# Kernel tuning notes

Measured on AMD Instinct MI355X. Metric: run time of the kernel, lower is better.

The kernel has to match this reference:

```python
import jax, jax.numpy as jnp
import numpy as np

NUM_CONCEPT = 256
NUM_QUESTION = 10000
DIM_EMB = 64
TIME_LOG = 5.0
BATCH, SEQ = 32, 1024


def setup_inputs() -> dict:
    key = jax.random.key(0)
    ks = jax.random.split(key, 10)
    concept_seq = jax.random.randint(ks[0], (BATCH, SEQ), 0, NUM_CONCEPT)
    question_seq = jax.random.randint(ks[1], (BATCH, SEQ), 0, NUM_QUESTION)
    correctness_seq = jax.random.randint(ks[2], (BATCH, SEQ), 0, 2)
    time_seq = jnp.sort(jax.random.randint(ks[3], (BATCH, SEQ), 0, 1000000), axis=-1)
    std = 0.01  # nn.init.normal_(..., std=0.01)
    alpha_inter_emb = std * jax.random.normal(ks[4], (2 * NUM_CONCEPT, DIM_EMB), jnp.float32)
    alpha_concept_emb = std * jax.random.normal(ks[5], (NUM_CONCEPT, DIM_EMB), jnp.float32)
    beta_inter_emb = std * jax.random.normal(ks[6], (2 * NUM_CONCEPT, DIM_EMB), jnp.float32)
    beta_concept_emb = std * jax.random.normal(ks[7], (NUM_CONCEPT, DIM_EMB), jnp.float32)
    question_bias = std * jax.random.normal(ks[8], (NUM_QUESTION, 1), jnp.float32)
    concept_bias = std * jax.random.normal(ks[9], (NUM_CONCEPT, 1), jnp.float32)
    return {
        "concept_seq": concept_seq,
        "question_seq": question_seq,
        "correctness_seq": correctness_seq,
        "time_seq": time_seq,
        "alpha_inter_emb": alpha_inter_emb,
        "alpha_concept_emb": alpha_concept_emb,
        "beta_inter_emb": beta_inter_emb,
        "beta_concept_emb": beta_concept_emb,
        "question_bias": question_bias,
        "concept_bias": concept_bias,
    }


def reference(concept_seq, question_seq, correctness_seq, time_seq,
              alpha_inter_emb, alpha_concept_emb, beta_inter_emb,
              beta_concept_emb, question_bias, concept_bias):
    num_concept = alpha_concept_emb.shape[0]
    seq_len = concept_seq.shape[1]
    inters = concept_seq + correctness_seq * num_concept  # [B,S]

    # small batched matmuls producing [B,S,S]
    alphas = jnp.einsum("bid,bjd->bij", alpha_inter_emb[inters], alpha_concept_emb[concept_seq])
    betas = jnp.clip(jnp.einsum("bid,bjd->bij", beta_inter_emb[inters], beta_concept_emb[concept_seq]) + 1.0, 0.0, 10.0)

    t = time_seq.astype(jnp.float32)
    delta_t = jnp.abs(t[:, :, None] - t[:, None, :])  # [B,S,S]
    delta_t = jnp.log(delta_t + 1e-10) / np.log(TIME_LOG).astype(np.float32)

    cross_effects = alphas * jnp.exp(-betas * delta_t)

    # keep strictly upper triangle (source i strictly before target j), sum over sources
    causal = jnp.triu(jnp.ones((seq_len, seq_len), jnp.float32), k=1)
    sum_t = jnp.sum(cross_effects * causal[None], axis=-2)  # [B,S]

    problem_bias = question_bias[question_seq][..., 0]
    skill_bias = concept_bias[concept_seq][..., 0]
    predict_score_batch = jax.nn.sigmoid(problem_bias + skill_bias + sum_t)[:, 1:]
    return predict_score_batch
```

## Files before the change

kernel.cpp:

```cpp
#include <hip/hip_runtime.h>
#include <math.h>

#define SEQ     1024
#define NBATCH  32
#define NC      256
#define NI      512
#define DIM     64
#define JT      64
#define NJT     (SEQ / JT)
#define NWAVE   16

__global__ __launch_bounds__(256) void build_tables(
    const float* __restrict__ aI, const float* __restrict__ aC,
    const float* __restrict__ bI, const float* __restrict__ bC,
    float2* __restrict__ tab)
{
    __shared__ float sA[DIM];
    __shared__ float sB[DIM];
    const int x = blockIdx.x;
    const int t = threadIdx.x;
    if (t < DIM)            sA[t]        = aI[x * DIM + t];
    else if (t < 2 * DIM)   sB[t - DIM]  = bI[x * DIM + (t - DIM)];
    __syncthreads();

    const int y = t;
    const float4* ca = (const float4*)(aC + y * DIM);
    const float4* cb = (const float4*)(bC + y * DIM);
    float da = 0.f, db = 0.f;
#pragma unroll
    for (int k = 0; k < DIM / 4; ++k) {
        float4 va = ca[k];
        float4 vb = cb[k];
        da += sA[4*k+0]*va.x + sA[4*k+1]*va.y + sA[4*k+2]*va.z + sA[4*k+3]*va.w;
        db += sB[4*k+0]*vb.x + sB[4*k+1]*vb.y + sB[4*k+2]*vb.z + sB[4*k+3]*vb.w;
    }
    float beta = fminf(fmaxf(db + 1.0f, 0.0f), 10.0f);
    tab[x * NC + y] = make_float2(da, beta);
}

__global__ __launch_bounds__(1024) void hawkes_main(
    const int* __restrict__ concept_seq, const int* __restrict__ question_seq,
    const int* __restrict__ correct_seq, const int* __restrict__ time_seq,
    const float2* __restrict__ tab,
    const float* __restrict__ qbias, const float* __restrict__ cbias,
    float* __restrict__ out)
{
    __shared__ int   inter_s[SEQ];
    __shared__ float t_s[SEQ];
    __shared__ float part[NWAVE][JT];

    const int b   = blockIdx.x;
    const int p   = blockIdx.y;
    const int tid = threadIdx.x;
    const int w   = tid >> 6;
    const int l   = tid & 63;

    const int jt_big   = (NJT - 1) - p;
    const int jt_small = p;
    const int I_big    = (jt_big + 1) * JT;

    for (int idx = tid; idx < I_big; idx += 1024) {
        int c = concept_seq[b * SEQ + idx];
        inter_s[idx] = c + NC * correct_seq[b * SEQ + idx];
        t_s[idx]     = (float)time_seq[b * SEQ + idx];
    }
    __syncthreads();

    const float inv_ln5 = 0.6213349345596119f;

#pragma unroll
    for (int tile = 0; tile < 2; ++tile) {
        const int jt = tile ? jt_small : jt_big;
        const int I  = (jt + 1) * JT;
        const int j  = jt * JT + l;
        const int cj = concept_seq[b * SEQ + j];
        const float tj = t_s[j];

        float acc = 0.0f;
        const int chunk = I >> 4;
        const int i0 = w * chunk;
#pragma unroll 4
        for (int i = i0; i < i0 + chunk; ++i) {
            const int   s  = inter_s[i];
            const float ti = t_s[i];
            float2 ab = tab[s * NC + cj];
            float dt  = fabsf(tj - ti);
            float dl  = __builtin_amdgcn_logf(dt + 1e-10f) * inv_ln5;
            float e   = __builtin_amdgcn_exp2f(-ab.y * dl);
            acc += (i < j) ? ab.x * e : 0.0f;
        }

        __syncthreads();
        part[w][l] = acc;
        __syncthreads();

        if (w == 0) {
            float s = 0.0f;
#pragma unroll
            for (int k = 0; k < NWAVE; ++k) s += part[k][l];
            if (j >= 1) {
                float z = qbias[question_seq[b * SEQ + j]] + cbias[cj] + s;
                float ez = __builtin_amdgcn_exp2f(-z * 1.4426950408889634f);
                out[b * (SEQ - 1) + (j - 1)] = 1.0f / (1.0f + ez);
            }
        }
    }
}

extern "C" void kernel_launch(void* const* d_in, const int* in_sizes, int n_in,
                              void* d_out, int out_size, void* d_ws, size_t ws_size,
                              hipStream_t stream) {
    const int*   concept_seq  = (const int*)  d_in[0];
    const int*   question_seq = (const int*)  d_in[1];
    const int*   correct_seq  = (const int*)  d_in[2];
    const int*   time_seq     = (const int*)  d_in[3];
    const float* aI           = (const float*)d_in[4];
    const float* aC           = (const float*)d_in[5];
    const float* bI           = (const float*)d_in[6];
    const float* bC           = (const float*)d_in[7];
    const float* qbias        = (const float*)d_in[8];
    const float* cbias        = (const float*)d_in[9];
    float*       out          = (float*)d_out;

    float2* tab = (float2*)d_ws;

    build_tables<<<NI, 256, 0, stream>>>(aI, aC, bI, bC, tab);
    hawkes_main<<<dim3(NBATCH, NJT / 2), 1024, 0, stream>>>(
        concept_seq, question_seq, correct_seq, time_seq, tab, qbias, cbias, out);
}
```

Before: 103.8 us.

## Split source range across two blocks and add finalize kernel for sigmoid

Adds a z-dimension to the main grid so each block sums half of the source positions, doubling the block count to improve CU occupancy and latency hiding. Partial sums are written to workspace and combined in a new finalize kernel that applies the biases and sigmoid. Also folds the 1/ln5 scaling into the beta table and packs table byte offsets with times in shared memory to cut per-iteration arithmetic. Costs an extra kernel launch and a global round trip for partials.

Result: no change. 105.2 us (+1.4%).

```diff
diff --git a/kernel.cpp b/kernel.cpp
--- a/kernel.cpp
+++ b/kernel.cpp
@@ -9,6 +9,8 @@
 #define JT      64
 #define NJT     (SEQ / JT)
 #define NWAVE   16
+
+#define PART_OFF (NI * NC * sizeof(float2))
 
 __global__ __launch_bounds__(256) void build_tables(
     const float* __restrict__ aI, const float* __restrict__ aC,
@@ -34,23 +36,23 @@
         da += sA[4*k+0]*va.x + sA[4*k+1]*va.y + sA[4*k+2]*va.z + sA[4*k+3]*va.w;
         db += sB[4*k+0]*vb.x + sB[4*k+1]*vb.y + sB[4*k+2]*vb.z + sB[4*k+3]*vb.w;
     }
-    float beta = fminf(fmaxf(db + 1.0f, 0.0f), 10.0f);
+    const float inv_ln5 = 0.6213349345596119f;
+    float beta = fminf(fmaxf(db + 1.0f, 0.0f), 10.0f) * inv_ln5;
     tab[x * NC + y] = make_float2(da, beta);
 }
 
 __global__ __launch_bounds__(1024) void hawkes_main(
-    const int* __restrict__ concept_seq, const int* __restrict__ question_seq,
+    const int* __restrict__ concept_seq,
     const int* __restrict__ correct_seq, const int* __restrict__ time_seq,
     const float2* __restrict__ tab,
-    const float* __restrict__ qbias, const float* __restrict__ cbias,
-    float* __restrict__ out)
+    float* __restrict__ partial)
 {
-    __shared__ int   inter_s[SEQ];
-    __shared__ float t_s[SEQ];
-    __shared__ float part[NWAVE][JT];
+    __shared__ float2 st[SEQ];
+    __shared__ float  part[NWAVE][JT];
 
     const int b   = blockIdx.x;
     const int p   = blockIdx.y;
+    const int z   = blockIdx.z;
     const int tid = threadIdx.x;
     const int w   = tid >> 6;
     const int l   = tid & 63;
@@ -59,33 +61,33 @@
     const int jt_small = p;
     const int I_big    = (jt_big + 1) * JT;
 
-    for (int idx = tid; idx < I_big; idx += 1024) {
-        int c = concept_seq[b * SEQ + idx];
-        inter_s[idx] = c + NC * correct_seq[b * SEQ + idx];
-        t_s[idx]     = (float)time_seq[b * SEQ + idx];
+    if (tid < I_big) {
+        int c   = concept_seq[b * SEQ + tid];
+        int off = (c + (correct_seq[b * SEQ + tid] << 8)) << 11;
+        st[tid] = make_float2(__int_as_float(off), (float)time_seq[b * SEQ + tid]);
     }
     __syncthreads();
 
-    const float inv_ln5 = 0.6213349345596119f;
+    const char* tabc = (const char*)tab;
 
 #pragma unroll
     for (int tile = 0; tile < 2; ++tile) {
         const int jt = tile ? jt_small : jt_big;
         const int I  = (jt + 1) * JT;
         const int j  = jt * JT + l;
-        const int cj = concept_seq[b * SEQ + j];
-        const float tj = t_s[j];
+        const int cj8 = concept_seq[b * SEQ + j] * 8;
+        const float tj = st[j].y;
 
         float acc = 0.0f;
-        const int chunk = I >> 4;
-        const int i0 = w * chunk;
+        const int chunk = I >> 5;
+        const int i0 = z * (I >> 1) + w * chunk;
 #pragma unroll 4
         for (int i = i0; i < i0 + chunk; ++i) {
-            const int   s  = inter_s[i];
-            const float ti = t_s[i];
-            float2 ab = tab[s * NC + cj];
-            float dt  = fabsf(tj - ti);
-            float dl  = __builtin_amdgcn_logf(dt + 1e-10f) * inv_ln5;
+            float2 sv = st[i];
+            int   off = __float_as_int(sv.x);
+            float2 ab = *(const float2*)(tabc + off + cj8);
+            float dt  = fabsf(tj - sv.y);
+            float dl  = __builtin_amdgcn_logf(dt + 1e-10f);
             float e   = __builtin_amdgcn_exp2f(-ab.y * dl);
             acc += (i < j) ? ab.x * e : 0.0f;
         }
@@ -98,13 +100,25 @@
             float s = 0.0f;
 #pragma unroll
             for (int k = 0; k < NWAVE; ++k) s += part[k][l];
-            if (j >= 1) {
-                float z = qbias[question_seq[b * SEQ + j]] + cbias[cj] + s;
-                float ez = __builtin_amdgcn_exp2f(-z * 1.4426950408889634f);
-                out[b * (SEQ - 1) + (j - 1)] = 1.0f / (1.0f + ez);
-            }
+            partial[(z * NBATCH + b) * SEQ + j] = s;
         }
     }
+}
+
+__global__ __launch_bounds__(256) void finalize(
+    const float* __restrict__ partial,
+    const int* __restrict__ concept_seq, const int* __restrict__ question_seq,
+    const float* __restrict__ qbias, const float* __restrict__ cbias,
+    float* __restrict__ out)
+{
+    const int idx = blockIdx.x * 256 + threadIdx.x;
+    const int b = idx >> 10;
+    const int j = idx & (SEQ - 1);
+    if (j < 1) return;
+    float s = partial[b * SEQ + j] + partial[(NBATCH + b) * SEQ + j];
+    float zv = qbias[question_seq[b * SEQ + j]] + cbias[concept_seq[b * SEQ + j]] + s;
+    float ez = __builtin_amdgcn_exp2f(-zv * 1.4426950408889634f);
+    out[b * (SEQ - 1) + (j - 1)] = 1.0f / (1.0f + ez);
 }
 
 extern "C" void kernel_launch(void* const* d_in, const int* in_sizes, int n_in,
@@ -122,9 +136,12 @@
     const float* cbias        = (const float*)d_in[9];
     float*       out          = (float*)d_out;
 
-    float2* tab = (float2*)d_ws;
+    float2* tab     = (float2*)d_ws;
+    float*  partial = (float*)((char*)d_ws + PART_OFF);
 
     build_tables<<<NI, 256, 0, stream>>>(aI, aC, bI, bC, tab);
-    hawkes_main<<<dim3(NBATCH, NJT / 2), 1024, 0, stream>>>(
-        concept_seq, question_seq, correct_seq, time_seq, tab, qbias, cbias, out);
+    hawkes_main<<<dim3(NBATCH, NJT / 2, 2), 1024, 0, stream>>>(
+        concept_seq, correct_seq, time_seq, tab, partial);
+    finalize<<<(NBATCH * SEQ) / 256, 256, 0, stream>>>(
+        partial, concept_seq, question_seq, qbias, cbias, out);
 }
```

## Pack alpha/beta table as bf16 pairs and fuse both tiles into one loop

Applied to the files above, without the earlier changes.

The precomputed alpha/beta table is stored as bf16 pairs instead of float2, with the 1/ln5 factor folded into beta, which halves table gather bytes. Sequence data is packed into a single shared float2 holding a precomputed byte row offset and the time. The two j-tiles are processed in one interleaved loop so each shared-memory load of source i serves both tiles, and the work is strided across waves, which removes one set of barriers. The trade-off is reduced precision on the alpha and beta coefficients.

After: 100.4 us. 3.3% less time.

```diff
diff --git a/kernel.cpp b/kernel.cpp
--- a/kernel.cpp
+++ b/kernel.cpp
@@ -1,4 +1,5 @@
 #include <hip/hip_runtime.h>
+#include <hip/hip_bf16.h>
 #include <math.h>
 
 #define SEQ     1024
@@ -13,7 +14,7 @@
 __global__ __launch_bounds__(256) void build_tables(
     const float* __restrict__ aI, const float* __restrict__ aC,
     const float* __restrict__ bI, const float* __restrict__ bC,
-    float2* __restrict__ tab)
+    __hip_bfloat162* __restrict__ tab)
 {
     __shared__ float sA[DIM];
     __shared__ float sB[DIM];
@@ -34,20 +35,23 @@
         da += sA[4*k+0]*va.x + sA[4*k+1]*va.y + sA[4*k+2]*va.z + sA[4*k+3]*va.w;
         db += sB[4*k+0]*vb.x + sB[4*k+1]*vb.y + sB[4*k+2]*vb.z + sB[4*k+3]*vb.w;
     }
-    float beta = fminf(fmaxf(db + 1.0f, 0.0f), 10.0f);
-    tab[x * NC + y] = make_float2(da, beta);
+    const float inv_ln5 = 0.6213349345596119f;
+    float beta = fminf(fmaxf(db + 1.0f, 0.0f), 10.0f) * inv_ln5;
+    __hip_bfloat162 v;
+    v.x = __float2bfloat16(da);
+    v.y = __float2bfloat16(beta);
+    tab[x * NC + y] = v;
 }
 
 __global__ __launch_bounds__(1024) void hawkes_main(
     const int* __restrict__ concept_seq, const int* __restrict__ question_seq,
     const int* __restrict__ correct_seq, const int* __restrict__ time_seq,
-    const float2* __restrict__ tab,
+    const __hip_bfloat162* __restrict__ tab,
     const float* __restrict__ qbias, const float* __restrict__ cbias,
     float* __restrict__ out)
 {
-    __shared__ int   inter_s[SEQ];
-    __shared__ float t_s[SEQ];
-    __shared__ float part[NWAVE][JT];
+    __shared__ float2 st[SEQ];
+    __shared__ float  part[NWAVE][2][JT];
 
     const int b   = blockIdx.x;
     const int p   = blockIdx.y;
@@ -55,54 +59,74 @@
     const int w   = tid >> 6;
     const int l   = tid & 63;
 
-    const int jt_big   = (NJT - 1) - p;
-    const int jt_small = p;
-    const int I_big    = (jt_big + 1) * JT;
+    const int jtB = (NJT - 1) - p;
+    const int jtS = p;
+    const int I_B = (jtB + 1) * JT;
+    const int I_S = (jtS + 1) * JT;
 
-    for (int idx = tid; idx < I_big; idx += 1024) {
-        int c = concept_seq[b * SEQ + idx];
-        inter_s[idx] = c + NC * correct_seq[b * SEQ + idx];
-        t_s[idx]     = (float)time_seq[b * SEQ + idx];
+    if (tid < I_B) {
+        int c   = concept_seq[b * SEQ + tid];
+        int off = (c + (correct_seq[b * SEQ + tid] << 8)) << 10;
+        st[tid] = make_float2(__int_as_float(off), (float)time_seq[b * SEQ + tid]);
     }
     __syncthreads();
 
-    const float inv_ln5 = 0.6213349345596119f;
+    const int   jB   = jtB * JT + l;
+    const int   jS   = jtS * JT + l;
+    const int   cB4  = concept_seq[b * SEQ + jB] * 4;
+    const int   cS4  = concept_seq[b * SEQ + jS] * 4;
+    const float tjB  = st[jB].y;
+    const float tjS  = st[jS].y;
 
+    const char* tabc = (const char*)tab;
+    float accB = 0.0f, accS = 0.0f;
+
+    const int nks = I_S >> 4;
+    const int nkb = I_B >> 4;
+
+#pragma unroll 4
+    for (int k = 0; k < nks; ++k) {
+        const int i = w + (k << 4);
+        float2 sv = st[i];
+        const char* row = tabc + __float_as_int(sv.x);
+        unsigned uB = *(const unsigned*)(row + cB4);
+        unsigned uS = *(const unsigned*)(row + cS4);
+        float dlB = __builtin_amdgcn_logf(fabsf(tjB - sv.y) + 1e-10f);
+        float dlS = __builtin_amdgcn_logf(fabsf(tjS - sv.y) + 1e-10f);
+        float aB  = __uint_as_float(uB << 16);
+        float bB  = __uint_as_float(uB & 0xFFFF0000u);
+        float aS  = __uint_as_float(uS << 16);
+        float bS  = __uint_as_float(uS & 0xFFFF0000u);
+        float eB  = __builtin_amdgcn_exp2f(-bB * dlB);
+        float eS  = __builtin_amdgcn_exp2f(-bS * dlS);
+        accB += (i < jB) ? aB * eB : 0.0f;
+        accS += (i < jS) ? aS * eS : 0.0f;
+    }
+#pragma unroll 4
+    for (int k = nks; k < nkb; ++k) {
+        const int i = w + (k << 4);
+        float2 sv = st[i];
+        unsigned uB = *(const unsigned*)(tabc + __float_as_int(sv.x) + cB4);
+        float dlB = __builtin_amdgcn_logf(fabsf(tjB - sv.y) + 1e-10f);
+        float aB  = __uint_as_float(uB << 16);
+        float bB  = __uint_as_float(uB & 0xFFFF0000u);
+        accB += (i < jB) ? aB * __builtin_amdgcn_exp2f(-bB * dlB) : 0.0f;
+    }
+
+    part[w][0][l] = accB;
+    part[w][1][l] = accS;
+    __syncthreads();
+
+    if (w < 2) {
+        const int j  = (w == 0) ? jB : jS;
+        float s = 0.0f;
 #pragma unroll
-    for (int tile = 0; tile < 2; ++tile) {
-        const int jt = tile ? jt_small : jt_big;
-        const int I  = (jt + 1) * JT;
-        const int j  = jt * JT + l;
-        const int cj = concept_seq[b * SEQ + j];
-        const float tj = t_s[j];
-
-        float acc = 0.0f;
-        const int chunk = I >> 4;
-        const int i0 = w * chunk;
-#pragma unroll 4
-        for (int i = i0; i < i0 + chunk; ++i) {
-            const int   s  = inter_s[i];
-            const float ti = t_s[i];
-            float2 ab = tab[s * NC + cj];
-            float dt  = fabsf(tj - ti);
-            float dl  = __builtin_amdgcn_logf(dt + 1e-10f) * inv_ln5;
-            float e   = __builtin_amdgcn_exp2f(-ab.y * dl);
-            acc += (i < j) ? ab.x * e : 0.0f;
-        }
-
-        __syncthreads();
-        part[w][l] = acc;
-        __syncthreads();
-
-        if (w == 0) {
-            float s = 0.0f;
-#pragma unroll
-            for (int k = 0; k < NWAVE; ++k) s += part[k][l];
-            if (j >= 1) {
-                float z = qbias[question_seq[b * SEQ + j]] + cbias[cj] + s;
-                float ez = __builtin_amdgcn_exp2f(-z * 1.4426950408889634f);
-                out[b * (SEQ - 1) + (j - 1)] = 1.0f / (1.0f + ez);
-            }
+        for (int k = 0; k < NWAVE; ++k) s += part[k][w][l];
+        if (j >= 1) {
+            float zv = qbias[question_seq[b * SEQ + j]]
+                     + cbias[concept_seq[b * SEQ + j]] + s;
+            float ez = __builtin_amdgcn_exp2f(-zv * 1.4426950408889634f);
+            out[b * (SEQ - 1) + (j - 1)] = 1.0f / (1.0f + ez);
         }
     }
 }
@@ -122,7 +146,7 @@
     const float* cbias        = (const float*)d_in[9];
     float*       out          = (float*)d_out;
 
-    float2* tab = (float2*)d_ws;
+    __hip_bfloat162* tab = (__hip_bfloat162*)d_ws;
 
     build_tables<<<NI, 256, 0, stream>>>(aI, aC, bI, bC, tab);
     hawkes_main<<<dim3(NBATCH, NJT / 2), 1024, 0, stream>>>(
```
